# Optimization experiments

Hardware: AMD Instinct MI355X
Metric: run time of the kernel (lower is better)

## Reference

```python
import jax, jax.numpy as jnp
import numpy as np

B, C, H, W = 16, 512, 32, 32

def _conv2d(x, w, b, pad):
    y = jax.lax.conv_general_dilated(
        x, w, window_strides=(1, 1), padding=[(pad, pad), (pad, pad)],
        dimension_numbers=('NCHW', 'OIHW', 'NCHW'))
    return y + b[None, :, None, None]

def setup_inputs() -> dict:
    key = jax.random.key(0)
    ks = jax.random.split(key, 10)
    s3 = 1.0 / np.sqrt(C * 9)   # torch conv2d default init scale (3x3)
    s1 = 1.0 / np.sqrt(3 * C)   # 1x1 conv over 3C input channels
    return {
        'x':  jax.random.normal(ks[0], (B, C, H, W), jnp.float32),
        'w1': jax.random.uniform(ks[1], (C, C, 3, 3), jnp.float32, -s3, s3),
        'b1': jax.random.uniform(ks[2], (C,), jnp.float32, -s3, s3),
        'w2': jax.random.uniform(ks[3], (C, C, 3, 3), jnp.float32, -s3, s3),
        'b2': jax.random.uniform(ks[4], (C,), jnp.float32, -s3, s3),
        'w3': jax.random.uniform(ks[5], (C, C, 3, 3), jnp.float32, -s3, s3),
        'b3': jax.random.uniform(ks[6], (C,), jnp.float32, -s3, s3),
        'alpha': jax.random.normal(ks[7], (), jnp.float32) * 0.1,
        'beta':  jax.random.normal(ks[8], (), jnp.float32) * 0.1,
        'wf': jax.random.uniform(ks[9], (C, 3 * C, 1, 1), jnp.float32, -s1, s1),
        'bf': jnp.zeros((C,), jnp.float32),
    }

def reference(x, w1, b1, w2, b2, w3, b3, alpha, beta, wf, bf):
    b, c, h, w = x.shape
    n = h * w
    # --- spatial attention ---
    A = _conv2d(x, w1, b1, 1).reshape(b, c, n)  # [b,C,N]
    Bm = _conv2d(x, w2, b2, 1).reshape(b, c, n)
    D = _conv2d(x, w3, b3, 1).reshape(b, c, n)
    M = jnp.einsum('bcn,bcm->bnm', A, Bm)       # A^T @ B, [b,N,N]
    M = jax.nn.softmax(M, axis=-1)
    # weighted_C = M @ D^T -> [b,N,C]; then permute to [b,C,N]
    spat = jnp.einsum('bnm,bcm->bcn', M, D).reshape(b, c, h, w)
    spat = alpha * spat
    # --- channel attention ---
    Xr = x.reshape(b, c, n)                     # [b,C,N]
    S = jnp.einsum('bcn,bdn->bcd', Xr, Xr)      # [b,C,C]
    S = jax.nn.softmax(S, axis=-1)
    # weighted = S^T @ Xr
    chan = jnp.einsum('bdc,bdn->bcn', S, Xr).reshape(b, c, h, w)
    chan = beta * chan
    # --- fuse ---
    cat = jnp.concatenate((x, spat, chan), axis=1)  # [b,3C,H,W]
    return _conv2d(cat, wf, bf, 0)
```

## Files before the change

kernel.cpp:

```cpp
#include <hip/hip_runtime.h>
#include <hip/hip_bf16.h>
#include <stdint.h>

#define B_   16
#define C_   512
#define N_   1024
#define C3   1536

using bf16x8 = __attribute__((ext_vector_type(8))) __bf16;
using f32x4  = __attribute__((ext_vector_type(4))) float;
typedef unsigned short ushort_t;

__device__ __forceinline__ ushort_t f2bf(float f) {
    union { float f; uint32_t u; } v; v.f = f;
    uint32_t r = v.u + 0x7FFFu + ((v.u >> 16) & 1u);
    return (ushort_t)(r >> 16);
}

typedef __attribute__((address_space(3))) void lds_void_t;
typedef const __attribute__((address_space(1))) void g_void_t;
__device__ __forceinline__ void gload16(const void* g, void* l) {
    __builtin_amdgcn_global_load_lds((g_void_t*)g, (lds_void_t*)l, 16, 0, 0);
}


__global__ void castwf_kernel(const float* __restrict__ wf,
                              ushort_t* __restrict__ Wfb,
                              ushort_t* __restrict__ zp,
                              const float* __restrict__ b1,
                              const float* __restrict__ b2,
                              const float* __restrict__ b3,
                              float* __restrict__ b_all) {
    int idx = blockIdx.x * 256 + threadIdx.x;
    if (idx < 512) zp[idx] = 0;
    if (idx < 1536) b_all[idx] = (idx < 512) ? b1[idx] : (idx < 1024) ? b2[idx - 512] : b3[idx - 1024];
    Wfb[idx] = f2bf(wf[idx]);
}

__global__ void castw_kernel(const float* __restrict__ w,
                             ushort_t* __restrict__ Wall, int coff) {
    int idx = blockIdx.x * 256 + threadIdx.x;
    int t = idx / (C_ * C_);
    int rem = idx - t * (C_ * C_);
    Wall[(size_t)t * (C3 * C_) + (size_t)coff * C_ + rem] = f2bf(w[(size_t)rem * 9 + t]);
}

__global__ void castx_kernel(const float* __restrict__ x,
                             ushort_t* __restrict__ Xb,
                             ushort_t* __restrict__ cat) {
    __shared__ ushort_t t[32][33];
    int n0 = blockIdx.x * 32, c0 = blockIdx.y * 32, b = blockIdx.z;
    int tx = threadIdx.x & 31, ty = threadIdx.x >> 5;
    const float* xb = x + ((size_t)b * C_ + c0) * N_ + n0;
#pragma unroll
    for (int q = 0; q < 4; ++q) {
        int c = ty + q * 8;
        ushort_t h = f2bf(xb[(size_t)c * N_ + tx]);
        Xb[((size_t)b * C_ + c0 + c) * N_ + n0 + tx] = h;
        t[c][tx] = h;
    }
    __syncthreads();
#pragma unroll
    for (int q = 0; q < 4; ++q) {
        int n = ty + q * 8;
        cat[((size_t)b * N_ + n0 + n) * C3 + c0 + tx] = t[tx][n];
    }
}

__global__ void transp_kernel(const ushort_t* __restrict__ Y,
                              ushort_t* __restrict__ Db) {
    __shared__ ushort_t t[32][33];
    int n0 = blockIdx.x * 32, c0 = blockIdx.y * 32, b = blockIdx.z;
    int tx = threadIdx.x & 31, ty = threadIdx.x >> 5;
#pragma unroll
    for (int q = 0; q < 4; ++q) {
        int n = ty + q * 8;
        t[n][tx] = Y[((size_t)b * N_ + n0 + n) * C3 + 1024 + c0 + tx];
    }
    __syncthreads();
#pragma unroll
    for (int q = 0; q < 4; ++q) {
        int c = ty + q * 8;
        Db[((size_t)b * C_ + c0 + c) * N_ + n0 + tx] = t[tx][c];
    }
}

__global__ void softmax_kernel(float* __restrict__ Mb) {
    int n = blockIdx.x, b = blockIdx.y;
    float* row = Mb + ((size_t)b * N_ + n) * N_;
    int tid = threadIdx.x;
    float4 v = ((const float4*)row)[tid];
    float m = fmaxf(fmaxf(v.x, v.y), fmaxf(v.z, v.w));
#pragma unroll
    for (int off = 1; off < 64; off <<= 1) m = fmaxf(m, __shfl_xor(m, off));
    __shared__ float sm[4], ss[4];
    int wid = tid >> 6, lane = tid & 63;
    if (lane == 0) sm[wid] = m;
    __syncthreads();
    m = fmaxf(fmaxf(sm[0], sm[1]), fmaxf(sm[2], sm[3]));
    float e0 = __expf(v.x - m), e1 = __expf(v.y - m);
    float e2 = __expf(v.z - m), e3 = __expf(v.w - m);
    float s = e0 + e1 + e2 + e3;
#pragma unroll
    for (int off = 1; off < 64; off <<= 1) s += __shfl_xor(s, off);
    if (lane == 0) ss[wid] = s;
    __syncthreads();
    s = ss[0] + ss[1] + ss[2] + ss[3];
    float r = 1.0f / s;
    ushort4 o;
    o.x = f2bf(e0 * r); o.y = f2bf(e1 * r); o.z = f2bf(e2 * r); o.w = f2bf(e3 * r);
    ((ushort4*)row)[tid] = o;
}

__global__ void rowstats_kernel(const float* __restrict__ S,
                                float* __restrict__ mxv, float* __restrict__ rzv) {
    int c = blockIdx.x, b = blockIdx.y;
    const float* row = S + ((size_t)b * C_ + c) * C_;
    int tid = threadIdx.x;
    float2 v = ((const float2*)row)[tid];
    float m = fmaxf(v.x, v.y);
#pragma unroll
    for (int off = 1; off < 64; off <<= 1) m = fmaxf(m, __shfl_xor(m, off));
    __shared__ float sm[4], ss[4];
    int wid = tid >> 6, lane = tid & 63;
    if (lane == 0) sm[wid] = m;
    __syncthreads();
    m = fmaxf(fmaxf(sm[0], sm[1]), fmaxf(sm[2], sm[3]));
    float e = __expf(v.x - m) + __expf(v.y - m);
#pragma unroll
    for (int off = 1; off < 64; off <<= 1) e += __shfl_xor(e, off);
    if (lane == 0) ss[wid] = e;
    __syncthreads();
    if (tid == 0) {
        e = ss[0] + ss[1] + ss[2] + ss[3];
        mxv[(size_t)b * C_ + c] = m;
        rzv[(size_t)b * C_ + c] = 1.0f / e;
    }
}

__global__ void sst_kernel(const float* __restrict__ S,
                           const float* __restrict__ mxv, const float* __restrict__ rzv,
                           ushort_t* __restrict__ Sst) {
    int idx = blockIdx.x * 256 + threadIdx.x;
    int d = idx & (C_ - 1);
    int b = idx >> 18;
    float st = mxv[((size_t)b << 9) + d];
    float rz = rzv[((size_t)b << 9) + d];
    Sst[idx] = f2bf(__expf(S[idx] - st) * rz);
}

#define BM 128
#define BN 128
#define BKk 64

template <int XMODE, int OUTF32, int BIASMODE, int SCALE, int SWZ>
__global__ __launch_bounds__(256)
void gemm_bt_kernel(const ushort_t* __restrict__ Ab, int lda, long long strideA, long long tapA,
                    const ushort_t* __restrict__ Bb, int ldb, long long strideB, long long tapB,
                    void* __restrict__ Cb, int ldc, long long strideC,
                    int K, int ntaps,
                    const float* __restrict__ bias,
                    const float* __restrict__ scaleptr,
                    const ushort_t* __restrict__ zpage) {
    __shared__ short As[BM * BKk];
    __shared__ short Bs[BN * BKk];
    int tid = threadIdx.x;
    int wid = tid >> 6, lane = tid & 63;
    int wr = wid >> 1, wc = wid & 1;
    int j0 = blockIdx.x * BN, i0 = blockIdx.y * BM, b = blockIdx.z;
    const ushort_t* Abase = Ab + (size_t)b * strideA;
    const ushort_t* Bbase = Bb + (size_t)b * strideB;

    f32x4 acc[4][4] = {};

    int rs = wid * 32 + (lane >> 3);
    int kb = (lane & 7) * 8;

    for (int tap = 0; tap < ntaps; ++tap) {
        const ushort_t* At_ = Abase + (size_t)tap * tapA;
        const ushort_t* Bt_ = Bbase + (size_t)tap * tapB;
        const ushort_t* aq[4];
        const ushort_t* bq[4];
#pragma unroll
        for (int q = 0; q < 4; ++q)
            aq[q] = At_ + (size_t)(i0 + rs + q * 8) * lda + kb;
#pragma unroll
        for (int q = 0; q < 4; ++q)
            bq[q] = Bt_ + (size_t)(j0 + rs + q * 8) * ldb + kb;

        for (int kk = 0; kk < K; kk += BKk) {
            __syncthreads();
#pragma unroll
            for (int q = 0; q < 4; ++q) {
                gload16(aq[q], &As[(wid * 32 + q * 8) * BKk]);
                aq[q] += BKk;
                gload16(bq[q], &Bs[(wid * 32 + q * 8) * BKk]);
                bq[q] += BKk;
            }
            __syncthreads();
#pragma unroll
            for (int kc = 0; kc < BKk; kc += 32) {
                bf16x8 af[4], bfr[4];
#pragma unroll
                for (int m = 0; m < 4; ++m)
                    af[m] = *(const bf16x8*)&As[(wr * 64 + m * 16 + (lane & 15)) * BKk + kc + (lane >> 4) * 8];
#pragma unroll
                for (int nb = 0; nb < 4; ++nb)
                    bfr[nb] = *(const bf16x8*)&Bs[(wc * 64 + nb * 16 + (lane & 15)) * BKk + kc + (lane >> 4) * 8];
#pragma unroll
                for (int m = 0; m < 4; ++m)
#pragma unroll
                    for (int nb = 0; nb < 4; ++nb)
                        acc[m][nb] = __builtin_amdgcn_mfma_f32_16x16x32_bf16(af[m], bfr[nb], acc[m][nb], 0, 0, 0);
            }
        }
    }

    float scale = SCALE ? *scaleptr : 1.0f;
#pragma unroll
    for (int m = 0; m < 4; ++m) {
#pragma unroll
        for (int nb = 0; nb < 4; ++nb) {
            int i = i0 + wr * 64 + m * 16 + (lane >> 4) * 4;
            int j = j0 + wc * 64 + nb * 16 + (lane & 15);
#pragma unroll
            for (int r = 0; r < 4; ++r) {
                float v = acc[m][nb][r];
                if (BIASMODE == 1) v += bias[i + r];
                if (BIASMODE == 2) v += bias[j];
                if (SCALE) v *= scale;
                if (OUTF32)
                    ((float*)Cb)[(size_t)b * strideC + (size_t)(i + r) * ldc + j] = v;
                else
                    ((ushort_t*)Cb)[(size_t)b * strideC + (size_t)(i + r) * ldc + j] = f2bf(v);
            }
        }
    }
}

#define R3BM 256
#define R3BN 128
#define R3BK 64

template <int XMODE, int OUTF32, int BIASMODE, int SCALE>
__global__ __launch_bounds__(512, 2)
void gemm_r3_kernel(const ushort_t* __restrict__ Ab, int lda, long long strideA, long long tapA,
                    const ushort_t* __restrict__ Bb, int ldb, long long strideB, long long tapB,
                    void* __restrict__ Cb, int ldc, long long strideC,
                    int K, int ntaps,
                    const float* __restrict__ bias,
                    const float* __restrict__ scaleptr,
                    const ushort_t* __restrict__ zpage) {
    __shared__ short As[3][R3BM * R3BK];
    __shared__ short Bs[3][R3BN * R3BK];
    int tid = threadIdx.x;
    int wid = tid >> 6, lane = tid & 63;
    int wr = wid >> 1, wc = wid & 1;
    int j0 = blockIdx.x * R3BN, i0 = blockIdx.y * R3BM, b = blockIdx.z;
    const ushort_t* Abase = Ab + (size_t)b * strideA;
    const ushort_t* Bbase = Bb + (size_t)b * strideB;
    int kpt = K >> 6;
    int nt = ntaps * kpt;

    f32x4 acc[4][4] = {};

    int sr = tid >> 3;
    int klds = (tid & 7) * 8;
    int sbase = wid * 512;

    int aoff[4][2], boff[4][2];
#pragma unroll
    for (int m = 0; m < 4; ++m) {
        int row = wr * 64 + m * 16 + (lane & 15);
        int sw = (row & 7) << 3;
#pragma unroll
        for (int h = 0; h < 2; ++h)
            aoff[m][h] = row * R3BK + ((h * 32 + (lane >> 4) * 8) ^ sw);
    }
#pragma unroll
    for (int nb = 0; nb < 4; ++nb) {
        int row = wc * 64 + nb * 16 + (lane & 15);
        int sw = (row & 7) << 3;
#pragma unroll
        for (int h = 0; h < 2; ++h)
            boff[nb][h] = row * R3BK + ((h * 32 + (lane >> 4) * 8) ^ sw);
    }

    const ushort_t* ap[4];
    const ushort_t* bp[2];
    int s_kk = 0, s_tap = 0;

    auto SETUP = [&](int tap) {
        const ushort_t* At_ = Abase + (size_t)tap * tapA;
        const ushort_t* Bt_ = Bbase + (size_t)tap * tapB;
        int dh = 0, dw = 0, nshift = 0;
        if (XMODE == 1) { dh = tap / 3 - 1; dw = tap - (tap / 3) * 3 - 1; nshift = dh * 32 + dw; }
#pragma unroll
        for (int s = 0; s < 4; ++s) {
            int r = sr + s * 64;
            int ks = klds ^ ((r & 7) << 3);
            if (XMODE == 1) {
                int n = i0 + r;
                int nn = n & (N_ - 1);
                int hh = (nn >> 5) + dh, ww = (nn & 31) + dw;
                bool valid = ((unsigned)hh < 32u) && ((unsigned)ww < 32u);
                ap[s] = valid ? (At_ + (size_t)(n + nshift) * lda + ks) : (zpage + ks);
            } else {
                ap[s] = At_ + (size_t)(i0 + r) * lda + ks;
            }
        }
#pragma unroll
        for (int s = 0; s < 2; ++s) {
            int r = sr + s * 64;
            int ks = klds ^ ((r & 7) << 3);
            bp[s] = Bt_ + (size_t)(j0 + r) * ldb + ks;
        }
    };

    auto STAGE = [&](int slot) {
#pragma unroll
        for (int s = 0; s < 4; ++s)
            gload16(ap[s], &As[slot][sbase + s * 4096]);
#pragma unroll
        for (int s = 0; s < 2; ++s)
            gload16(bp[s], &Bs[slot][sbase + s * 4096]);
        if (++s_kk == kpt) {
            s_kk = 0;
            if (++s_tap < ntaps) SETUP(s_tap);
        } else {
#pragma unroll
            for (int s = 0; s < 4; ++s) ap[s] += R3BK;
#pragma unroll
            for (int s = 0; s < 2; ++s) bp[s] += R3BK;
        }
    };

    SETUP(0);
    STAGE(0);
    STAGE(1);

    for (int t = 0; t < nt; ++t) {
        int slot = t - (t / 3) * 3;
        if (t + 1 < nt) asm volatile("s_waitcnt vmcnt(6)" ::: "memory");
        else            asm volatile("s_waitcnt vmcnt(0)" ::: "memory");
        __builtin_amdgcn_s_barrier();
        __builtin_amdgcn_sched_barrier(0);

        const short* Aslot = &As[slot][0];
        const short* Bslot = &Bs[slot][0];
        bf16x8 af[4][2], bfr[4][2];
#pragma unroll
        for (int h = 0; h < 2; ++h) {
#pragma unroll
            for (int m = 0; m < 4; ++m)
                af[m][h] = *(const bf16x8*)&Aslot[aoff[m][h]];
#pragma unroll
            for (int nb = 0; nb < 4; ++nb)
                bfr[nb][h] = *(const bf16x8*)&Bslot[boff[nb][h]];
        }

        if (t + 2 < nt) STAGE((t + 2) - ((t + 2) / 3) * 3);

        asm volatile("s_waitcnt lgkmcnt(8)" ::: "memory");
        __builtin_amdgcn_sched_barrier(0);
        __builtin_amdgcn_s_setprio(1);
#pragma unroll
        for (int m = 0; m < 4; ++m)
#pragma unroll
            for (int nb = 0; nb < 4; ++nb)
                acc[m][nb] = __builtin_amdgcn_mfma_f32_16x16x32_bf16(af[m][0], bfr[nb][0], acc[m][nb], 0, 0, 0);
        asm volatile("s_waitcnt lgkmcnt(0)" ::: "memory");
        __builtin_amdgcn_sched_barrier(0);
#pragma unroll
        for (int m = 0; m < 4; ++m)
#pragma unroll
            for (int nb = 0; nb < 4; ++nb)
                acc[m][nb] = __builtin_amdgcn_mfma_f32_16x16x32_bf16(af[m][1], bfr[nb][1], acc[m][nb], 0, 0, 0);
        __builtin_amdgcn_s_setprio(0);
    }

    float scale = SCALE ? *scaleptr : 1.0f;
#pragma unroll
    for (int m = 0; m < 4; ++m) {
#pragma unroll
        for (int nb = 0; nb < 4; ++nb) {
            int i = i0 + wr * 64 + m * 16 + (lane >> 4) * 4;
            int j = j0 + wc * 64 + nb * 16 + (lane & 15);
#pragma unroll
            for (int r = 0; r < 4; ++r) {
                float v = acc[m][nb][r];
                if (BIASMODE == 1) v += bias[i + r];
                if (BIASMODE == 2) v += bias[j];
                if (SCALE) v *= scale;
                if (OUTF32)
                    ((float*)Cb)[(size_t)b * strideC + (size_t)(i + r) * ldc + j] = v;
                else
                    ((ushort_t*)Cb)[(size_t)b * strideC + (size_t)(i + r) * ldc + j] = f2bf(v);
            }
        }
    }
}

constexpr size_t OFF_ZP   = 0;
constexpr size_t OFF_BALL = 1024;
constexpr size_t OFF_WFB  = OFF_BALL + 6144;
constexpr size_t OFF_CAT  = OFF_WFB + (size_t)C_ * C3 * 2;
constexpr size_t OFF_Y    = OFF_CAT + (size_t)B_ * N_ * C3 * 2;
constexpr size_t OFF_DB   = OFF_Y + (size_t)B_ * N_ * C3 * 2;
constexpr size_t OFF_SR   = OFF_DB + (size_t)B_ * C_ * N_ * 2;
constexpr size_t OFF_SST  = OFF_SR + (size_t)B_ * C_ * C_ * 4;
constexpr size_t OFF_MX   = OFF_SST + (size_t)B_ * C_ * C_ * 2;
constexpr size_t OFF_RZ   = OFF_MX + (size_t)B_ * C_ * 4;
constexpr size_t OFF_U    = OFF_RZ + (size_t)B_ * C_ * 4;
constexpr size_t OFF_WALL = OFF_U;
constexpr size_t OFF_XB   = OFF_U + (size_t)9 * C3 * C_ * 2;
constexpr size_t OFF_M    = OFF_U;
constexpr size_t EXT_A    = OFF_XB + (size_t)B_ * C_ * N_ * 2;
constexpr size_t EXT_B    = OFF_M + (size_t)B_ * N_ * N_ * 4;
constexpr size_t WS_NEED  = EXT_A > EXT_B ? EXT_A : EXT_B;

extern "C" void kernel_launch(void* const* d_in, const int* in_sizes, int n_in,
                              void* d_out, int out_size, void* d_ws, size_t ws_size,
                              hipStream_t stream) {
    const float* x   = (const float*)d_in[0];
    const float* w1  = (const float*)d_in[1];
    const float* b1  = (const float*)d_in[2];
    const float* w2  = (const float*)d_in[3];
    const float* b2  = (const float*)d_in[4];
    const float* w3  = (const float*)d_in[5];
    const float* b3  = (const float*)d_in[6];
    const float* alpha = (const float*)d_in[7];
    const float* beta  = (const float*)d_in[8];
    const float* wf  = (const float*)d_in[9];
    const float* bfv = (const float*)d_in[10];
    float* out = (float*)d_out;
    char* ws = (char*)d_ws;
    if (ws_size < WS_NEED) return;

    ushort_t* zp   = (ushort_t*)(ws + OFF_ZP);
    float*    ball = (float*)(ws + OFF_BALL);
    ushort_t* Wfb  = (ushort_t*)(ws + OFF_WFB);
    ushort_t* cat  = (ushort_t*)(ws + OFF_CAT);
    ushort_t* Y    = (ushort_t*)(ws + OFF_Y);
    ushort_t* Db   = (ushort_t*)(ws + OFF_DB);
    float*    Sr   = (float*)(ws + OFF_SR);
    ushort_t* Sst  = (ushort_t*)(ws + OFF_SST);
    float*    mxv  = (float*)(ws + OFF_MX);
    float*    rzv  = (float*)(ws + OFF_RZ);
    ushort_t* Wall = (ushort_t*)(ws + OFF_WALL);
    ushort_t* Xb   = (ushort_t*)(ws + OFF_XB);
    float*    Mb   = (float*)(ws + OFF_M);

    castwf_kernel<<<(C_ * C3) / 256, 256, 0, stream>>>(wf, Wfb, zp, b1, b2, b3, ball);
    castw_kernel<<<(9 * C_ * C_) / 256, 256, 0, stream>>>(w1, Wall, 0);
    castw_kernel<<<(9 * C_ * C_) / 256, 256, 0, stream>>>(w2, Wall, 512);
    castw_kernel<<<(9 * C_ * C_) / 256, 256, 0, stream>>>(w3, Wall, 1024);
    castx_kernel<<<dim3(N_ / 32, C_ / 32, B_), 256, 0, stream>>>(x, Xb, cat);

    for (int c = 0; c < 3; ++c) {
        gemm_r3_kernel<1, 0, 2, 0><<<dim3(4, 64, 1), 512, 0, stream>>>(
            cat, C3, 0, 0,
            Wall + (size_t)c * 512 * C_, C_, 0, (long long)C3 * C_,
            Y + (size_t)c * 512, C3, 0,
            C_, 9, ball + c * 512, nullptr, zp);
    }
    transp_kernel<<<dim3(N_ / 32, C_ / 32, B_), 256, 0, stream>>>(Y, Db);
    gemm_bt_kernel<0, 1, 0, 0, 0><<<dim3(4, 4, B_), 256, 0, stream>>>(
        Xb, N_, (long long)C_ * N_, 0,
        Xb, N_, (long long)C_ * N_, 0,
        Sr, C_, (long long)C_ * C_,
        N_, 1, nullptr, nullptr, zp);
    rowstats_kernel<<<dim3(C_, B_), 256, 0, stream>>>(Sr, mxv, rzv);
    sst_kernel<<<(B_ * C_ * C_) / 256, 256, 0, stream>>>(Sr, mxv, rzv, Sst);
    gemm_r3_kernel<0, 1, 0, 0><<<dim3(8, 4, B_), 512, 0, stream>>>(
        Y, C3, (long long)N_ * C3, 0,
        Y + 512, C3, (long long)N_ * C3, 0,
        Mb, N_, (long long)N_ * N_,
        C_, 1, nullptr, nullptr, zp);
    softmax_kernel<<<dim3(N_, B_), 256, 0, stream>>>(Mb);
    gemm_r3_kernel<0, 0, 0, 1><<<dim3(4, 4, B_), 512, 0, stream>>>(
        (const ushort_t*)Mb, 2048, (long long)N_ * 2048, 0,
        Db, N_, (long long)C_ * N_, 0,
        cat + 512, C3, (long long)N_ * C3,
        N_, 1, nullptr, alpha, zp);
    gemm_r3_kernel<0, 0, 0, 1><<<dim3(4, 4, B_), 512, 0, stream>>>(
        cat, C3, (long long)N_ * C3, 0,
        Sst, C_, (long long)C_ * C_, 0,
        cat + 1024, C3, (long long)N_ * C3,
        C_, 1, nullptr, beta, zp);
    gemm_r3_kernel<0, 1, 1, 0><<<dim3(8, 2, B_), 512, 0, stream>>>(
        Wfb, C3, 0, 0,
        cat, C3, (long long)N_ * C3, 0,
        out, N_, (long long)C_ * N_,
        C3, 1, bfv, nullptr, zp);
}
```

Measured before the change: 480.5 us.

## Use zero-padded spatial input buffer for 3x3 conv GEMM and reorder tap loop

```diff
diff --git a/kernel.cpp b/kernel.cpp
--- a/kernel.cpp
+++ b/kernel.cpp
@@ -6,6 +6,7 @@
 #define C_   512
 #define N_   1024
 #define C3   1536
+#define NPAD 1156
 
 using bf16x8 = __attribute__((ext_vector_type(8))) __bf16;
 using f32x4  = __attribute__((ext_vector_type(4))) float;
@@ -47,7 +48,8 @@
 
 __global__ void castx_kernel(const float* __restrict__ x,
                              ushort_t* __restrict__ Xb,
-                             ushort_t* __restrict__ cat) {
+                             ushort_t* __restrict__ cat,
+                             ushort_t* __restrict__ catP) {
     __shared__ ushort_t t[32][33];
     int n0 = blockIdx.x * 32, c0 = blockIdx.y * 32, b = blockIdx.z;
     int tx = threadIdx.x & 31, ty = threadIdx.x >> 5;
@@ -63,7 +65,10 @@
 #pragma unroll
     for (int q = 0; q < 4; ++q) {
         int n = ty + q * 8;
-        cat[((size_t)b * N_ + n0 + n) * C3 + c0 + tx] = t[tx][n];
+        ushort_t v = t[tx][n];
+        cat[((size_t)b * N_ + n0 + n) * C3 + c0 + tx] = v;
+        int prow = (n0 >> 5) * 34 + n + 35;
+        catP[((size_t)b * NPAD + prow) * C_ + c0 + tx] = v;
     }
 }
 
@@ -257,8 +262,6 @@
     int wid = tid >> 6, lane = tid & 63;
     int wr = wid >> 1, wc = wid & 1;
     int j0 = blockIdx.x * R3BN, i0 = blockIdx.y * R3BM, b = blockIdx.z;
-    const ushort_t* Abase = Ab + (size_t)b * strideA;
-    const ushort_t* Bbase = Bb + (size_t)b * strideB;
     int kpt = K >> 6;
     int nt = ntaps * kpt;
 
@@ -286,56 +289,46 @@
             boff[nb][h] = row * R3BK + ((h * 32 + (lane >> 4) * 8) ^ sw);
     }
 
-    const ushort_t* ap[4];
-    const ushort_t* bp[2];
-    int s_kk = 0, s_tap = 0;
-
-    auto SETUP = [&](int tap) {
-        const ushort_t* At_ = Abase + (size_t)tap * tapA;
-        const ushort_t* Bt_ = Bbase + (size_t)tap * tapB;
-        int dh = 0, dw = 0, nshift = 0;
-        if (XMODE == 1) { dh = tap / 3 - 1; dw = tap - (tap / 3) * 3 - 1; nshift = dh * 32 + dw; }
-#pragma unroll
-        for (int s = 0; s < 4; ++s) {
-            int r = sr + s * 64;
-            int ks = klds ^ ((r & 7) << 3);
-            if (XMODE == 1) {
-                int n = i0 + r;
-                int nn = n & (N_ - 1);
-                int hh = (nn >> 5) + dh, ww = (nn & 31) + dw;
-                bool valid = ((unsigned)hh < 32u) && ((unsigned)ww < 32u);
-                ap[s] = valid ? (At_ + (size_t)(n + nshift) * lda + ks) : (zpage + ks);
-            } else {
-                ap[s] = At_ + (size_t)(i0 + r) * lda + ks;
-            }
-        }
-#pragma unroll
-        for (int s = 0; s < 2; ++s) {
-            int r = sr + s * 64;
-            int ks = klds ^ ((r & 7) << 3);
-            bp[s] = Bt_ + (size_t)(j0 + r) * ldb + ks;
-        }
+    const ushort_t* pa[4];
+    const ushort_t* pb[2];
+#pragma unroll
+    for (int s = 0; s < 4; ++s) {
+        int r = sr + s * 64;
+        int ks = klds ^ ((r & 7) << 3);
+        if (XMODE == 1) {
+            int li = (i0 & (N_ - 1)) + r;
+            int pr = (li >> 5) * 34 + (li & 31) + 35;
+            pa[s] = Ab + ((size_t)(i0 >> 10) * NPAD + pr) * lda + ks;
+        } else {
+            pa[s] = Ab + (size_t)b * strideA + (size_t)(i0 + r) * lda + ks;
+        }
+    }
+#pragma unroll
+    for (int s = 0; s < 2; ++s) {
+        int r = sr + s * 64;
+        int ks = klds ^ ((r & 7) << 3);
+        pb[s] = Bb + (size_t)b * strideB + (size_t)(j0 + r) * ldb + ks;
+    }
+
+    int s_tap = 0, s_kk = 0;
+    auto STAGE = [&](int slot) {
+        long long uA, uB;
+        if (XMODE == 1) {
+            int dh = s_tap / 3 - 1, dw = s_tap - (s_tap / 3) * 3 - 1;
+            uA = (long long)(dh * 34 + dw) * lda + s_kk * R3BK;
+        } else {
+            uA = (long long)s_tap * tapA + (long long)s_kk * R3BK;
+        }
+        uB = (long long)s_tap * tapB + (long long)s_kk * R3BK;
+#pragma unroll
+        for (int s = 0; s < 4; ++s)
+            gload16(pa[s] + uA, &As[slot][sbase + s * 4096]);
+#pragma unroll
+        for (int s = 0; s < 2; ++s)
+            gload16(pb[s] + uB, &Bs[slot][sbase + s * 4096]);
+        if (++s_tap == ntaps) { s_tap = 0; ++s_kk; }
     };
 
-    auto STAGE = [&](int slot) {
-#pragma unroll
-        for (int s = 0; s < 4; ++s)
-            gload16(ap[s], &As[slot][sbase + s * 4096]);
-#pragma unroll
-        for (int s = 0; s < 2; ++s)
-            gload16(bp[s], &Bs[slot][sbase + s * 4096]);
-        if (++s_kk == kpt) {
-            s_kk = 0;
-            if (++s_tap < ntaps) SETUP(s_tap);
-        } else {
-#pragma unroll
-            for (int s = 0; s < 4; ++s) ap[s] += R3BK;
-#pragma unroll
-            for (int s = 0; s < 2; ++s) bp[s] += R3BK;
-        }
-    };
-
-    SETUP(0);
     STAGE(0);
     STAGE(1);
 
@@ -412,10 +405,14 @@
 constexpr size_t OFF_MX   = OFF_SST + (size_t)B_ * C_ * C_ * 2;
 constexpr size_t OFF_RZ   = OFF_MX + (size_t)B_ * C_ * 4;
 constexpr size_t OFF_U    = OFF_RZ + (size_t)B_ * C_ * 4;
+constexpr size_t WALL_SZ  = (size_t)9 * C3 * C_ * 2;
+constexpr size_t XB_SZ    = (size_t)B_ * C_ * N_ * 2;
+constexpr size_t CATP_SZ  = (size_t)B_ * NPAD * C_ * 2;
 constexpr size_t OFF_WALL = OFF_U;
-constexpr size_t OFF_XB   = OFF_U + (size_t)9 * C3 * C_ * 2;
+constexpr size_t OFF_XB   = OFF_U + WALL_SZ;
+constexpr size_t OFF_CATP = OFF_XB + XB_SZ;
 constexpr size_t OFF_M    = OFF_U;
-constexpr size_t EXT_A    = OFF_XB + (size_t)B_ * C_ * N_ * 2;
+constexpr size_t EXT_A    = OFF_CATP + CATP_SZ;
 constexpr size_t EXT_B    = OFF_M + (size_t)B_ * N_ * N_ * 4;
 constexpr size_t WS_NEED  = EXT_A > EXT_B ? EXT_A : EXT_B;
 
@@ -449,17 +446,20 @@
     float*    rzv  = (float*)(ws + OFF_RZ);
     ushort_t* Wall = (ushort_t*)(ws + OFF_WALL);
     ushort_t* Xb   = (ushort_t*)(ws + OFF_XB);
+    ushort_t* catP = (ushort_t*)(ws + OFF_CATP);
     float*    Mb   = (float*)(ws + OFF_M);
+
+    hipMemsetAsync(catP, 0, CATP_SZ, stream);
 
     castwf_kernel<<<(C_ * C3) / 256, 256, 0, stream>>>(wf, Wfb, zp, b1, b2, b3, ball);
     castw_kernel<<<(9 * C_ * C_) / 256, 256, 0, stream>>>(w1, Wall, 0);
     castw_kernel<<<(9 * C_ * C_) / 256, 256, 0, stream>>>(w2, Wall, 512);
     castw_kernel<<<(9 * C_ * C_) / 256, 256, 0, stream>>>(w3, Wall, 1024);
-    castx_kernel<<<dim3(N_ / 32, C_ / 32, B_), 256, 0, stream>>>(x, Xb, cat);
+    castx_kernel<<<dim3(N_ / 32, C_ / 32, B_), 256, 0, stream>>>(x, Xb, cat, catP);
 
     for (int c = 0; c < 3; ++c) {
         gemm_r3_kernel<1, 0, 2, 0><<<dim3(4, 64, 1), 512, 0, stream>>>(
-            cat, C3, 0, 0,
+            catP, C_, 0, 0,
             Wall + (size_t)c * 512 * C_, C_, 0, (long long)C3 * C_,
             Y + (size_t)c * 512, C3, 0,
             C_, 9, ball + c * 512, nullptr, zp);
```

Result: faster. 445.9 us (-7.2%).
